# Optimization experiments

Measured on AMD Instinct MI355X. Metric: run time of the kernel, lower is better.

Reference implementation:

```python
import jax, jax.numpy as jnp
import numpy as np

N_HEAD = 16
HEAD_DIM = 64
EPS = 1e-5
ROPE_BASE = 10000.0


def setup_inputs() -> dict:
    key = jax.random.key(0)
    ks = jax.random.split(key, 3)
    B, T, C = 4, 2048, 1024
    x = jax.random.normal(ks[0], (B, T, C), dtype=jnp.float32)
    Wqkv = jax.random.normal(ks[1], (C, 3 * C), dtype=jnp.float32) * (C ** -0.5)
    Wproj = jax.random.normal(ks[2], (C, C), dtype=jnp.float32) * (C ** -0.5)
    q_norm_w = jnp.ones((HEAD_DIM,), dtype=jnp.float32)
    k_norm_w = jnp.ones((HEAD_DIM,), dtype=jnp.float32)
    return {"x": x, "Wqkv": Wqkv, "Wproj": Wproj, "q_norm_w": q_norm_w, "k_norm_w": k_norm_w}


def _rms_norm(x, w):
    xf = x.astype(jnp.float32)
    normed = xf * jax.lax.rsqrt(jnp.mean(xf * xf, axis=-1, keepdims=True) + EPS)
    return (normed * w).astype(x.dtype)


def _rope_tables(T, dtype):
    inv_freq = 1.0 / (ROPE_BASE ** (jnp.arange(0, HEAD_DIM, 2, dtype=jnp.float32) / HEAD_DIM))
    t = jnp.arange(T, dtype=jnp.float32)
    freqs = jnp.outer(t, inv_freq)              # [T, D/2]
    emb = jnp.concatenate([freqs, freqs], -1)   # [T, D]
    return jnp.cos(emb).astype(dtype), jnp.sin(emb).astype(dtype)


def _rotate_half(x):
    x1, x2 = jnp.split(x, 2, axis=-1)
    return jnp.concatenate([-x2, x1], axis=-1)


def reference(x, Wqkv, Wproj, q_norm_w, k_norm_w):
    B, T, C = x.shape
    qkv = x @ Wqkv                               # [B, T, 3C]
    q, k, v = jnp.split(qkv, 3, axis=-1)
    # [B, H, T, D]
    q = q.reshape(B, T, N_HEAD, HEAD_DIM).transpose(0, 2, 1, 3)
    k = k.reshape(B, T, N_HEAD, HEAD_DIM).transpose(0, 2, 1, 3)
    v = v.reshape(B, T, N_HEAD, HEAD_DIM).transpose(0, 2, 1, 3)
    # per-head QK RMSNorm
    q = _rms_norm(q, q_norm_w)
    k = _rms_norm(k, k_norm_w)
    # RoPE
    cos, sin = _rope_tables(T, q.dtype)          # [T, D] broadcast over B,H
    q = q * cos + _rotate_half(q) * sin
    k = k * cos + _rotate_half(k) * sin
    # causal attention
    scale = 1.0 / np.sqrt(HEAD_DIM)
    att = jnp.einsum('bhqd,bhkd->bhqk', q, k) * scale
    causal = jnp.tril(jnp.ones((T, T), dtype=bool))
    att = jnp.where(causal, att, -jnp.inf)
    att = jax.nn.softmax(att, axis=-1)
    y = jnp.einsum('bhqk,bhkd->bhqd', att, v)    # [B, H, T, D]
    y = y.transpose(0, 2, 1, 3).reshape(B, T, C)
    return y @ Wproj
```

## Files before the change

kernel.cpp:

```cpp
#include <hip/hip_runtime.h>
#include <cstdint>
#include <type_traits>

typedef __attribute__((ext_vector_type(8))) short bf16x8;
typedef __attribute__((ext_vector_type(4))) float f32x4;

typedef unsigned int __attribute__((address_space(1))) as1_uint;
typedef unsigned int __attribute__((address_space(3))) as3_uint;

__device__ __forceinline__ void llds16(const void* g, void* l) {
  __builtin_amdgcn_global_load_lds((const as1_uint*)g, (as3_uint*)l, 16, 0, 0);
}

__device__ __forceinline__ unsigned short f2bf(float f) {
  unsigned int u = __builtin_bit_cast(unsigned int, f);
  u = (u + 0x7fffu + ((u >> 16) & 1u)) >> 16;
  return (unsigned short)u;
}
__device__ __forceinline__ float bf2f(unsigned short h) {
  unsigned int u = ((unsigned int)h) << 16;
  return __builtin_bit_cast(float, u);
}

#define MEMBAR() asm volatile("" ::: "memory")

__global__ __launch_bounds__(256) void cvt_f32_bf16(const float* __restrict__ in,
                                                    unsigned short* __restrict__ out, int n4) {
  int i = blockIdx.x * blockDim.x + threadIdx.x;
  int stride = gridDim.x * blockDim.x;
  for (; i < n4; i += stride) {
    float4 v = ((const float4*)in)[i];
    uint2 p;
    p.x = (unsigned)f2bf(v.x) | ((unsigned)f2bf(v.y) << 16);
    p.y = (unsigned)f2bf(v.z) | ((unsigned)f2bf(v.w) << 16);
    ((uint2*)out)[i] = p;
  }
}

__global__ __launch_bounds__(256) void transpose_f32_bf16(const float* __restrict__ W,
                                                          unsigned short* __restrict__ Wt,
                                                          int K, int N) {
  __shared__ float tile[64][65];
  int n0 = blockIdx.x * 64, k0 = blockIdx.y * 64;
  int t = threadIdx.x;
  int lr = t >> 4, lc = (t & 15) * 4;
#pragma unroll
  for (int i = 0; i < 4; ++i) {
    int k = lr + i * 16;
    float4 v = *(const float4*)&W[(size_t)(k0 + k) * N + n0 + lc];
    tile[k][lc] = v.x; tile[k][lc + 1] = v.y; tile[k][lc + 2] = v.z; tile[k][lc + 3] = v.w;
  }
  __syncthreads();
  int n = t >> 2, kc = (t & 3) * 16;
  unsigned short* dst = &Wt[(size_t)(n0 + n) * K + k0 + kc];
#pragma unroll
  for (int j = 0; j < 16; ++j) dst[j] = f2bf(tile[kc + j][n]);
}

__global__ __launch_bounds__(256) void rope_tabT(float* __restrict__ cosT, float* __restrict__ sinT) {
  int i = blockIdx.x * 256 + threadIdx.x;
  int dm = i >> 11, t = i & 2047;
  float inv = powf(10000.0f, -(float)dm * (1.0f / 32.0f));
  float a = (float)t * inv;
  cosT[i] = cosf(a);
  sinT[i] = sinf(a);
}

__device__ __forceinline__ void block_map(int& bx, int& by) {
  const int lin = blockIdx.y * gridDim.x + blockIdx.x;
  const int xcd = lin & 7;
  const int idx = lin >> 3;
  const int ych = gridDim.y >> 3;
  by = xcd * ych + (idx & (ych - 1));
  bx = idx / ych;
}

template <typename OutT>
__global__ __launch_bounds__(256) void gemm_ring(const unsigned short* __restrict__ A,
                                                 const unsigned short* __restrict__ Bt,
                                                 OutT* __restrict__ C, int M, int N, int K) {
  __shared__ unsigned short As[3][128 * 32];
  __shared__ unsigned short Bs[3][128 * 32];
  const int tid = threadIdx.x;
  const int w = tid >> 6, lane = tid & 63;
  const int l15 = lane & 15, lg = lane >> 4;
  const int wr = w >> 1, wc = w & 1;

  int bx, by;
  block_map(bx, by);
  const int m0 = by * 128, n0 = bx * 128;

  const size_t K2 = (size_t)K * 2;
  const char* Ag = (const char*)A;
  const char* Bg = (const char*)Bt;
  const int rc = lane >> 2;
  const int cb = (lane & 3) * 16;

  auto stage = [&](int buf, int kt) {
#pragma unroll
    for (int i = 0; i < 2; ++i) {
      int c = w + i * 4;
      int row = c * 16 + rc;
      int srcc = cb ^ (((row >> 1) & 3) << 4);
      size_t kofs = (size_t)kt * 64 + srcc;
      llds16(Ag + (size_t)(m0 + row) * K2 + kofs, (char*)&As[buf][0] + c * 1024);
      llds16(Bg + (size_t)(n0 + row) * K2 + kofs, (char*)&Bs[buf][0] + c * 1024);
    }
  };

  f32x4 acc[4][4] = {};
  const int nk = K >> 5;
  stage(0, 0);
  stage(1, 1);
  int cur = 0;
  for (int t = 0; t < nk; ++t) {
    if (t + 1 < nk) asm volatile("s_waitcnt vmcnt(4)" ::: "memory");
    else            asm volatile("s_waitcnt vmcnt(0)" ::: "memory");
    __builtin_amdgcn_s_barrier();
    MEMBAR();
    if (t + 2 < nk) stage(cur + 2 >= 3 ? cur - 1 : cur + 2, t + 2);

    const unsigned short* Ab = &As[cur][0];
    const unsigned short* Bb = &Bs[cur][0];
    bf16x8 af[4], bfr[4];
#pragma unroll
    for (int m = 0; m < 4; ++m) {
      int row = wr * 64 + m * 16 + l15;
      af[m] = *(const bf16x8*)((const char*)Ab + row * 64 + ((lg * 16) ^ (((row >> 1) & 3) << 4)));
    }
#pragma unroll
    for (int n = 0; n < 4; ++n) {
      int row = wc * 64 + n * 16 + l15;
      bfr[n] = *(const bf16x8*)((const char*)Bb + row * 64 + ((lg * 16) ^ (((row >> 1) & 3) << 4)));
    }
#pragma unroll
    for (int m = 0; m < 4; ++m)
#pragma unroll
      for (int n = 0; n < 4; ++n)
        acc[m][n] = __builtin_amdgcn_mfma_f32_16x16x32_bf16(af[m], bfr[n], acc[m][n], 0, 0, 0);
    cur = (cur == 2) ? 0 : cur + 1;
  }

#pragma unroll
  for (int m = 0; m < 4; ++m)
#pragma unroll
    for (int n = 0; n < 4; ++n) {
      int row = m0 + wr * 64 + m * 16 + lg * 4;
      int col = n0 + wc * 64 + n * 16 + l15;
#pragma unroll
      for (int r = 0; r < 4; ++r) {
        if constexpr (std::is_same<OutT, float>::value)
          C[(size_t)(row + r) * N + col] = acc[m][n][r];
        else
          C[(size_t)(row + r) * N + col] = f2bf(acc[m][n][r]);
      }
    }
}

__global__ __launch_bounds__(256, 2) void gemm_qkvW(const unsigned short* __restrict__ A,
                                                    const unsigned short* __restrict__ Bt,
                                                    const float* __restrict__ qw,
                                                    const float* __restrict__ kw,
                                                    const float* __restrict__ cosTT,
                                                    const float* __restrict__ sinTT,
                                                    unsigned short* __restrict__ Qr,
                                                    unsigned short* __restrict__ Kr,
                                                    unsigned short* __restrict__ Vtg) {
  constexpr int K = 1024;
  constexpr int nk = K >> 5;
  __shared__ unsigned short smem[36864];
  char* base = (char*)smem;

  const int tid = threadIdx.x;
  const int w = tid >> 6, lane = tid & 63;
  const int l15 = lane & 15, lg = lane >> 4;
  const int wr = w >> 1, wc = w & 1;

  int bx, by;
  block_map(bx, by);
  const int m0 = by * 256, n0 = bx * 128;

  const size_t K2 = (size_t)K * 2;
  const char* Ag = (const char*)A;
  const char* Bg = (const char*)Bt;
  const int rc4 = tid >> 2;
  const int cb = (tid & 3) * 16;

  auto stage = [&](int buf, int kt) {
    char* ab = base + buf * 24576;
#pragma unroll
    for (int j = 0; j < 4; ++j) {
      int row = j * 64 + rc4;
      int srcc = cb ^ (((row >> 1) & 3) << 4);
      llds16(Ag + (size_t)(m0 + row) * K2 + (size_t)kt * 64 + srcc,
             ab + j * 4096 + tid * 16);
    }
#pragma unroll
    for (int j = 0; j < 2; ++j) {
      int row = j * 64 + rc4;
      int srcc = cb ^ (((row >> 1) & 3) << 4);
      llds16(Bg + (size_t)(n0 + row) * K2 + (size_t)kt * 64 + srcc,
             ab + 16384 + j * 4096 + tid * 16);
    }
  };

  f32x4 acc[8][4] = {};
  stage(0, 0);
  stage(1, 1);
  int cur = 0;
  for (int t = 0; t < nk; ++t) {
    if (t + 1 < nk) asm volatile("s_waitcnt vmcnt(6)" ::: "memory");
    else            asm volatile("s_waitcnt vmcnt(0)" ::: "memory");
    __builtin_amdgcn_s_barrier();
    MEMBAR();
    if (t + 2 < nk) stage(cur + 2 >= 3 ? cur - 1 : cur + 2, t + 2);

    const char* Ab = base + cur * 24576;
    const char* Bb = Ab + 16384;
    bf16x8 af[8], bfr[4];
#pragma unroll
    for (int m = 0; m < 8; ++m) {
      int row = wr * 128 + m * 16 + l15;
      af[m] = *(const bf16x8*)(Ab + row * 64 + ((lg * 16) ^ (((row >> 1) & 3) << 4)));
    }
#pragma unroll
    for (int n = 0; n < 4; ++n) {
      int row = wc * 64 + n * 16 + l15;
      bfr[n] = *(const bf16x8*)(Bb + row * 64 + ((lg * 16) ^ (((row >> 1) & 3) << 4)));
    }
    __builtin_amdgcn_s_setprio(1);
#pragma unroll
    for (int m = 0; m < 8; ++m)
#pragma unroll
      for (int n = 0; n < 4; ++n)
        acc[m][n] = __builtin_amdgcn_mfma_f32_16x16x32_bf16(af[m], bfr[n], acc[m][n], 0, 0, 0);
    __builtin_amdgcn_s_setprio(0);
    cur = (cur == 2) ? 0 : cur + 1;
  }

  __syncthreads();

  const int head2 = bx * 2 + wc;
  const int cls = head2 >> 4;
  const int head = head2 & 15;
  const int rowb = m0 + wr * 128;
  const int b = rowb >> 11;
  const int tl = rowb & 2047;
  const int bh = b * 16 + head;
  unsigned short* tb = smem + w * 4864;

  if (cls < 2) {
    const float* wt = cls ? kw : qw;
    const float scale = cls ? 1.0f : 0.18033688011112042f;
    unsigned short* outp = cls ? Kr : Qr;
    float wv[4];
#pragma unroll
    for (int n = 0; n < 4; ++n) wv[n] = wt[n * 16 + l15];
    const float* c0p = cosTT + l15 * 2048;
    const float* c1p = cosTT + (16 + l15) * 2048;
    const float* s0p = sinTT + l15 * 2048;
    const float* s1p = sinTT + (16 + l15) * 2048;
#pragma unroll
    for (int chunk = 0; chunk < 2; ++chunk) {
#pragma unroll
      for (int q = 0; q < 4; ++q) {
        const int m = chunk * 4 + q;
        int t0 = tl + m * 16 + lg * 4;
        f32x4 ssq = {};
#pragma unroll
        for (int n = 0; n < 4; ++n) ssq += acc[m][n] * acc[m][n];
#pragma unroll
        for (int r = 0; r < 4; ++r) {
          float v = ssq[r];
          v += __shfl_xor(v, 1); v += __shfl_xor(v, 2);
          v += __shfl_xor(v, 4); v += __shfl_xor(v, 8);
          ssq[r] = rsqrtf(v * (1.0f / 64.0f) + 1e-5f) * scale;
        }
        f32x4 nv[4];
#pragma unroll
        for (int n = 0; n < 4; ++n) nv[n] = acc[m][n] * ssq * wv[n];
        f32x4 cv0 = *(const f32x4*)(c0p + t0);
        f32x4 cv1 = *(const f32x4*)(c1p + t0);
        f32x4 sv0 = *(const f32x4*)(s0p + t0);
        f32x4 sv1 = *(const f32x4*)(s1p + t0);
        f32x4 ov[4];
        ov[0] = nv[0] * cv0 - nv[2] * sv0;
        ov[1] = nv[1] * cv1 - nv[3] * sv1;
        ov[2] = nv[2] * cv0 + nv[0] * sv0;
        ov[3] = nv[3] * cv1 + nv[1] * sv1;
        int tloc = q * 16 + lg * 4;
#pragma unroll
        for (int n = 0; n < 4; ++n)
#pragma unroll
          for (int r = 0; r < 4; ++r)
            tb[(tloc + r) * 76 + n * 16 + l15] = f2bf(ov[n][r]);
      }
      MEMBAR();
      const int t = lane;
      unsigned short* yp = outp + ((size_t)bh * 2048 + tl + chunk * 64 + t) * 64;
#pragma unroll
      for (int j = 0; j < 8; ++j)
        *(bf16x8*)(yp + j * 8) = *(const bf16x8*)(tb + t * 76 + j * 8);
      MEMBAR();
    }
  } else {
#pragma unroll
    for (int chunk = 0; chunk < 2; ++chunk) {
#pragma unroll
      for (int q = 0; q < 4; ++q) {
        const int m = chunk * 4 + q;
#pragma unroll
        for (int n = 0; n < 4; ++n) {
          int d = n * 16 + l15, tloc = q * 16 + lg * 4;
          ushort4 pk;
          pk.x = f2bf(acc[m][n][0]); pk.y = f2bf(acc[m][n][1]);
          pk.z = f2bf(acc[m][n][2]); pk.w = f2bf(acc[m][n][3]);
          *(ushort4*)(tb + d * 76 + tloc) = pk;
        }
      }
      MEMBAR();
      int d2 = lane;
      unsigned short* vp = Vtg + ((size_t)bh * 64 + d2) * 2048 + tl + chunk * 64;
#pragma unroll
      for (int j = 0; j < 8; ++j) {
        bf16x8 vv = *(const bf16x8*)(tb + d2 * 76 + j * 8);
        *(bf16x8*)(vp + j * 8) = vv;
      }
      MEMBAR();
    }
  }
}

__global__ __launch_bounds__(256) void attn_fwd(const unsigned short* __restrict__ Q,
                                                const unsigned short* __restrict__ K,
                                                const unsigned short* __restrict__ Vtg,
                                                unsigned short* __restrict__ Y) {
  const int bh = blockIdx.x;
  const int pr = blockIdx.y;
  const int b = bh >> 4, h = bh & 15;
  const int tid = threadIdx.x;
  const int w = tid >> 6, lane = tid & 63;
  const int l15 = lane & 15, lg = lane >> 4;

  __shared__ unsigned short Kl[2][64 * 64];
  __shared__ unsigned short Vt[2][64 * 64];
  __shared__ unsigned short Pl[4][16 * 64];

  const size_t bhT = (size_t)bh * 2048;
  const char* Kg = (const char*)(K + bhT * 64);
  const char* Vg = (const char*)(Vtg + bhT * 64);

  auto stage = [&](int buf, int kt) {
#pragma unroll
    for (int i = 0; i < 2; ++i) {
      int c = w * 2 + i;
      int pos = c * 1024 + lane * 16;
      int row = pos >> 7, cb = pos & 127;
      int srcb = cb ^ ((row & 7) << 4);
      llds16(Kg + ((size_t)(kt * 64 + row)) * 128 + srcb,
             (char*)&Kl[buf][0] + c * 1024);
      llds16(Vg + (size_t)row * 4096 + (size_t)kt * 128 + srcb,
             (char*)&Vt[buf][0] + c * 1024);
    }
  };

  auto run_qtile = [&](int qtb) {
    const int qbase = qtb * 64;
    const unsigned short* Qp = Q + (bhT + qbase + w * 16 + l15) * 64 + lg * 8;
    bf16x8 aq[2];
    aq[0] = *(const bf16x8*)(Qp);
    aq[1] = *(const bf16x8*)(Qp + 32);

    f32x4 o[4] = {};
    float psum = 0.0f;

    char* Pw = (char*)&Pl[w][0];
    const int psw = (l15 & 7) << 4;

    for (int kt = 0; kt <= qtb; ++kt) {
      const int cur = kt & 1;
      if (kt < qtb) stage(cur ^ 1, kt + 1);
      const char* Kc = (const char*)&Kl[cur][0];
      const char* Vc = (const char*)&Vt[cur][0];

      f32x4 s[4] = {};
      __builtin_amdgcn_s_setprio(1);
#pragma unroll
      for (int n = 0; n < 4; ++n) {
        int r = n * 16 + l15, sw = (r & 7) << 4;
#pragma unroll
        for (int ks = 0; ks < 2; ++ks) {
          bf16x8 bk = *(const bf16x8*)(Kc + r * 128 + ((ks * 64 + lg * 16) ^ sw));
          s[n] = __builtin_amdgcn_mfma_f32_16x16x32_bf16(bk, aq[ks], s[n], 0, 0, 0);
        }
      }
      __builtin_amdgcn_s_setprio(0);

      if (kt == qtb) {
#pragma unroll
        for (int n = 0; n < 4; ++n)
#pragma unroll
          for (int r = 0; r < 4; ++r)
            if (n * 16 + lg * 4 + r > w * 16 + l15) s[n][r] = -1e30f;
      }

#pragma unroll
      for (int n = 0; n < 4; ++n) {
        float p0 = __builtin_exp2f(s[n][0]);
        float p1 = __builtin_exp2f(s[n][1]);
        float p2 = __builtin_exp2f(s[n][2]);
        float p3 = __builtin_exp2f(s[n][3]);
        psum += (p0 + p1) + (p2 + p3);
        unsigned u0 = __builtin_bit_cast(unsigned, p0);
        unsigned u1 = __builtin_bit_cast(unsigned, p1);
        unsigned u2 = __builtin_bit_cast(unsigned, p2);
        unsigned u3 = __builtin_bit_cast(unsigned, p3);
        uint2 pk;
        pk.x = (u0 >> 16) | (u1 & 0xffff0000u);
        pk.y = (u2 >> 16) | (u3 & 0xffff0000u);
        *(uint2*)(Pw + l15 * 128 + ((n * 32 + lg * 8) ^ psw)) = pk;
      }
      MEMBAR();

      bf16x8 ap[2];
      ap[0] = *(const bf16x8*)(Pw + l15 * 128 + ((lg * 16) ^ psw));
      ap[1] = *(const bf16x8*)(Pw + l15 * 128 + ((64 + lg * 16) ^ psw));

      __builtin_amdgcn_s_setprio(1);
#pragma unroll
      for (int df = 0; df < 4; ++df) {
        int rr = df * 16 + l15, sw = (rr & 7) << 4;
#pragma unroll
        for (int ks = 0; ks < 2; ++ks) {
          bf16x8 bv = *(const bf16x8*)(Vc + rr * 128 + ((ks * 64 + lg * 16) ^ sw));
          o[df] = __builtin_amdgcn_mfma_f32_16x16x32_bf16(bv, ap[ks], o[df], 0, 0, 0);
        }
      }
      __builtin_amdgcn_s_setprio(0);
      __syncthreads();
    }

    psum += __shfl_xor(psum, 16);
    psum += __shfl_xor(psum, 32);
    float inv = 1.0f / psum;

    size_t q = qbase + w * 16 + l15;
    unsigned short* yp = Y + ((size_t)b * 2048 + q) * 1024 + h * 64 + lg * 4;
#pragma unroll
    for (int df = 0; df < 4; ++df) {
      ushort4 v;
      v.x = f2bf(o[df][0] * inv);
      v.y = f2bf(o[df][1] * inv);
      v.z = f2bf(o[df][2] * inv);
      v.w = f2bf(o[df][3] * inv);
      *(ushort4*)(yp + df * 16) = v;
    }
  };

  stage(0, 0);
  __syncthreads();
  run_qtile(31 - pr);
  stage(0, 0);
  __syncthreads();
  run_qtile(pr);
}

extern "C" void kernel_launch(void* const* d_in, const int* in_sizes, int n_in,
                              void* d_out, int out_size, void* d_ws, size_t ws_size,
                              hipStream_t stream) {
  const float* x = (const float*)d_in[0];
  const float* Wqkv = (const float*)d_in[1];
  const float* Wproj = (const float*)d_in[2];
  const float* qw = (const float*)d_in[3];
  const float* kw = (const float*)d_in[4];
  float* out = (float*)d_out;

  char* ws = (char*)d_ws;
  unsigned short* xb = (unsigned short*)ws;        ws += (size_t)8192 * 1024 * 2;
  unsigned short* wqkvt = (unsigned short*)ws;     ws += (size_t)3072 * 1024 * 2;
  unsigned short* wprojt = (unsigned short*)ws;    ws += (size_t)1024 * 1024 * 2;
  unsigned short* Qr = (unsigned short*)ws;        ws += (size_t)64 * 2048 * 64 * 2;
  unsigned short* Kr = (unsigned short*)ws;        ws += (size_t)64 * 2048 * 64 * 2;
  unsigned short* Vtg = (unsigned short*)ws;       ws += (size_t)64 * 64 * 2048 * 2;
  unsigned short* yb = (unsigned short*)ws;        ws += (size_t)8192 * 1024 * 2;
  float* cosTT = (float*)ws;                       ws += (size_t)32 * 2048 * 4;
  float* sinTT = (float*)ws;                       ws += (size_t)32 * 2048 * 4;

  cvt_f32_bf16<<<2048, 256, 0, stream>>>(x, xb, 8192 * 1024 / 4);
  transpose_f32_bf16<<<dim3(48, 16), 256, 0, stream>>>(Wqkv, wqkvt, 1024, 3072);
  transpose_f32_bf16<<<dim3(16, 16), 256, 0, stream>>>(Wproj, wprojt, 1024, 1024);
  rope_tabT<<<256, 256, 0, stream>>>(cosTT, sinTT);
  gemm_qkvW<<<dim3(24, 32), 256, 0, stream>>>(xb, wqkvt, qw, kw, cosTT, sinTT, Qr, Kr, Vtg);
  attn_fwd<<<dim3(64, 16), 256, 0, stream>>>(Qr, Kr, Vtg, yb);
  gemm_ring<float><<<dim3(8, 64), 256, 0, stream>>>(yb, wprojt, out, 8192, 1024, 1024);
}
```

Baseline: 185.8 us.

## Enlarge attention query tile to 128 rows with 32 rows per wave

The attention kernel now processes 128-query tiles, with each wave handling two 16-row MFMA slices. Each K/V fragment read from LDS feeds two MFMAs, halving LDS traffic per FLOP and halving K/V staging per query row. The grid shrinks to 64x8 blocks, and each wave skips fully masked key tiles via the dq check. The cost is more registers per wave, a larger P buffer in LDS, fewer blocks for occupancy, and some waves idling at the causal diagonal.

```diff
diff --git a/kernel.cpp b/kernel.cpp
--- a/kernel.cpp
+++ b/kernel.cpp
@@ -344,7 +344,7 @@
 
   __shared__ unsigned short Kl[2][64 * 64];
   __shared__ unsigned short Vt[2][64 * 64];
-  __shared__ unsigned short Pl[4][16 * 64];
+  __shared__ unsigned short Pl[4][32 * 64];
 
   const size_t bhT = (size_t)bh * 2048;
   const char* Kg = (const char*)(K + bhT * 64);
@@ -364,102 +364,126 @@
     }
   };
 
-  auto run_qtile = [&](int qtb) {
-    const int qbase = qtb * 64;
-    const unsigned short* Qp = Q + (bhT + qbase + w * 16 + l15) * 64 + lg * 8;
-    bf16x8 aq[2];
-    aq[0] = *(const bf16x8*)(Qp);
-    aq[1] = *(const bf16x8*)(Qp + 32);
-
-    f32x4 o[4] = {};
-    float psum = 0.0f;
+  auto run_qtile = [&](int j) {
+    const int qbase = j * 128;
+    bf16x8 aq[2][2];
+#pragma unroll
+    for (int mi = 0; mi < 2; ++mi) {
+      const unsigned short* Qp = Q + (bhT + qbase + w * 32 + mi * 16 + l15) * 64 + lg * 8;
+      aq[mi][0] = *(const bf16x8*)(Qp);
+      aq[mi][1] = *(const bf16x8*)(Qp + 32);
+    }
+
+    f32x4 o[2][4] = {};
+    float psum[2] = {};
 
     char* Pw = (char*)&Pl[w][0];
     const int psw = (l15 & 7) << 4;
 
-    for (int kt = 0; kt <= qtb; ++kt) {
+    const int ktmax = 2 * j + 1;
+    for (int kt = 0; kt <= ktmax; ++kt) {
       const int cur = kt & 1;
-      if (kt < qtb) stage(cur ^ 1, kt + 1);
-      const char* Kc = (const char*)&Kl[cur][0];
-      const char* Vc = (const char*)&Vt[cur][0];
-
-      f32x4 s[4] = {};
-      __builtin_amdgcn_s_setprio(1);
-#pragma unroll
-      for (int n = 0; n < 4; ++n) {
-        int r = n * 16 + l15, sw = (r & 7) << 4;
-#pragma unroll
-        for (int ks = 0; ks < 2; ++ks) {
-          bf16x8 bk = *(const bf16x8*)(Kc + r * 128 + ((ks * 64 + lg * 16) ^ sw));
-          s[n] = __builtin_amdgcn_mfma_f32_16x16x32_bf16(bk, aq[ks], s[n], 0, 0, 0);
+      if (kt < ktmax) stage(cur ^ 1, kt + 1);
+      const int dq = qbase + w * 32 - kt * 64;
+
+      if (dq > -32) {
+        const char* Kc = (const char*)&Kl[cur][0];
+        const char* Vc = (const char*)&Vt[cur][0];
+
+        f32x4 s[2][4] = {};
+        __builtin_amdgcn_s_setprio(1);
+#pragma unroll
+        for (int n = 0; n < 4; ++n) {
+          int r = n * 16 + l15, sw = (r & 7) << 4;
+#pragma unroll
+          for (int ks = 0; ks < 2; ++ks) {
+            bf16x8 bk = *(const bf16x8*)(Kc + r * 128 + ((ks * 64 + lg * 16) ^ sw));
+#pragma unroll
+            for (int mi = 0; mi < 2; ++mi)
+              s[mi][n] = __builtin_amdgcn_mfma_f32_16x16x32_bf16(bk, aq[mi][ks], s[mi][n], 0, 0, 0);
+          }
         }
+        __builtin_amdgcn_s_setprio(0);
+
+        if (dq < 63) {
+#pragma unroll
+          for (int mi = 0; mi < 2; ++mi) {
+            int qv = dq + mi * 16 + l15;
+#pragma unroll
+            for (int n = 0; n < 4; ++n)
+#pragma unroll
+              for (int r = 0; r < 4; ++r)
+                if (n * 16 + lg * 4 + r > qv) s[mi][n][r] = -1e30f;
+          }
+        }
+
+#pragma unroll
+        for (int mi = 0; mi < 2; ++mi)
+#pragma unroll
+          for (int n = 0; n < 4; ++n) {
+            float p0 = __builtin_exp2f(s[mi][n][0]);
+            float p1 = __builtin_exp2f(s[mi][n][1]);
+            float p2 = __builtin_exp2f(s[mi][n][2]);
+            float p3 = __builtin_exp2f(s[mi][n][3]);
+            psum[mi] += (p0 + p1) + (p2 + p3);
+            unsigned u0 = __builtin_bit_cast(unsigned, p0);
+            unsigned u1 = __builtin_bit_cast(unsigned, p1);
+            unsigned u2 = __builtin_bit_cast(unsigned, p2);
+            unsigned u3 = __builtin_bit_cast(unsigned, p3);
+            uint2 pk;
+            pk.x = (u0 >> 16) | (u1 & 0xffff0000u);
+            pk.y = (u2 >> 16) | (u3 & 0xffff0000u);
+            *(uint2*)(Pw + (mi * 16 + l15) * 128 + ((n * 32 + lg * 8) ^ psw)) = pk;
+          }
+        MEMBAR();
+
+        bf16x8 ap[2][2];
+#pragma unroll
+        for (int mi = 0; mi < 2; ++mi)
+#pragma unroll
+          for (int ks = 0; ks < 2; ++ks)
+            ap[mi][ks] = *(const bf16x8*)(Pw + (mi * 16 + l15) * 128 + ((ks * 64 + lg * 16) ^ psw));
+
+        __builtin_amdgcn_s_setprio(1);
+#pragma unroll
+        for (int df = 0; df < 4; ++df) {
+          int rr = df * 16 + l15, sw = (rr & 7) << 4;
+#pragma unroll
+          for (int ks = 0; ks < 2; ++ks) {
+            bf16x8 bv = *(const bf16x8*)(Vc + rr * 128 + ((ks * 64 + lg * 16) ^ sw));
+#pragma unroll
+            for (int mi = 0; mi < 2; ++mi)
+              o[mi][df] = __builtin_amdgcn_mfma_f32_16x16x32_bf16(bv, ap[mi][ks], o[mi][df], 0, 0, 0);
+          }
+        }
+        __builtin_amdgcn_s_setprio(0);
       }
-      __builtin_amdgcn_s_setprio(0);
-
-      if (kt == qtb) {
-#pragma unroll
-        for (int n = 0; n < 4; ++n)
-#pragma unroll
-          for (int r = 0; r < 4; ++r)
-            if (n * 16 + lg * 4 + r > w * 16 + l15) s[n][r] = -1e30f;
+      __syncthreads();
+    }
+
+#pragma unroll
+    for (int mi = 0; mi < 2; ++mi) {
+      float l = psum[mi];
+      l += __shfl_xor(l, 16);
+      l += __shfl_xor(l, 32);
+      float inv = 1.0f / l;
+      size_t q = qbase + w * 32 + mi * 16 + l15;
+      unsigned short* yp = Y + ((size_t)b * 2048 + q) * 1024 + h * 64 + lg * 4;
+#pragma unroll
+      for (int df = 0; df < 4; ++df) {
+        ushort4 v;
+        v.x = f2bf(o[mi][df][0] * inv);
+        v.y = f2bf(o[mi][df][1] * inv);
+        v.z = f2bf(o[mi][df][2] * inv);
+        v.w = f2bf(o[mi][df][3] * inv);
+        *(ushort4*)(yp + df * 16) = v;
       }
-
-#pragma unroll
-      for (int n = 0; n < 4; ++n) {
-        float p0 = __builtin_exp2f(s[n][0]);
-        float p1 = __builtin_exp2f(s[n][1]);
-        float p2 = __builtin_exp2f(s[n][2]);
-        float p3 = __builtin_exp2f(s[n][3]);
-        psum += (p0 + p1) + (p2 + p3);
-        unsigned u0 = __builtin_bit_cast(unsigned, p0);
-        unsigned u1 = __builtin_bit_cast(unsigned, p1);
-        unsigned u2 = __builtin_bit_cast(unsigned, p2);
-        unsigned u3 = __builtin_bit_cast(unsigned, p3);
-        uint2 pk;
-        pk.x = (u0 >> 16) | (u1 & 0xffff0000u);
-        pk.y = (u2 >> 16) | (u3 & 0xffff0000u);
-        *(uint2*)(Pw + l15 * 128 + ((n * 32 + lg * 8) ^ psw)) = pk;
-      }
-      MEMBAR();
-
-      bf16x8 ap[2];
-      ap[0] = *(const bf16x8*)(Pw + l15 * 128 + ((lg * 16) ^ psw));
-      ap[1] = *(const bf16x8*)(Pw + l15 * 128 + ((64 + lg * 16) ^ psw));
-
-      __builtin_amdgcn_s_setprio(1);
-#pragma unroll
-      for (int df = 0; df < 4; ++df) {
-        int rr = df * 16 + l15, sw = (rr & 7) << 4;
-#pragma unroll
-        for (int ks = 0; ks < 2; ++ks) {
-          bf16x8 bv = *(const bf16x8*)(Vc + rr * 128 + ((ks * 64 + lg * 16) ^ sw));
-          o[df] = __builtin_amdgcn_mfma_f32_16x16x32_bf16(bv, ap[ks], o[df], 0, 0, 0);
-        }
-      }
-      __builtin_amdgcn_s_setprio(0);
-      __syncthreads();
-    }
-
-    psum += __shfl_xor(psum, 16);
-    psum += __shfl_xor(psum, 32);
-    float inv = 1.0f / psum;
-
-    size_t q = qbase + w * 16 + l15;
-    unsigned short* yp = Y + ((size_t)b * 2048 + q) * 1024 + h * 64 + lg * 4;
-#pragma unroll
-    for (int df = 0; df < 4; ++df) {
-      ushort4 v;
-      v.x = f2bf(o[df][0] * inv);
-      v.y = f2bf(o[df][1] * inv);
-      v.z = f2bf(o[df][2] * inv);
-      v.w = f2bf(o[df][3] * inv);
-      *(ushort4*)(yp + df * 16) = v;
     }
   };
 
   stage(0, 0);
   __syncthreads();
-  run_qtile(31 - pr);
+  run_qtile(15 - pr);
   stage(0, 0);
   __syncthreads();
   run_qtile(pr);
@@ -491,6 +515,6 @@
   transpose_f32_bf16<<<dim3(16, 16), 256, 0, stream>>>(Wproj, wprojt, 1024, 1024);
   rope_tabT<<<256, 256, 0, stream>>>(cosTT, sinTT);
   gemm_qkvW<<<dim3(24, 32), 256, 0, stream>>>(xb, wqkvt, qw, kw, cosTT, sinTT, Qr, Kr, Vtg);
-  attn_fwd<<<dim3(64, 16), 256, 0, stream>>>(Qr, Kr, Vtg, yb);
+  attn_fwd<<<dim3(64, 8), 256, 0, stream>>>(Qr, Kr, Vtg, yb);
   gemm_ring<float><<<dim3(8, 64), 256, 0, stream>>>(yb, wprojt, out, 8192, 1024, 1024);
 }
```

Measured after the change: 192.3 us. 1.04x slower.
